# Kernel optimization log

Measured on AMD Instinct MI355X. Metric: run time of the kernel, lower is better.

Reference implementation:

```python
import jax
jax.config.update("jax_enable_x64", True)  # Sinkhorn runs in f64, matching torch's d.double()
import jax.numpy as jnp
import numpy as np

N, D, K = 32768, 128, 1024
TAU = 0.2
SK_EPS = 0.005
SK_ITERS = 3


def setup_inputs() -> dict:
    key = jax.random.key(0)
    k1, k2 = jax.random.split(key)
    x = jax.random.normal(k1, (N, D), dtype=jnp.float32)
    codebook = jax.random.normal(k2, (K, D), dtype=jnp.float32) * 0.02  # embedding.weight
    return {"x": x, "codebook": codebook}


def _l2norm(v):
    # F.normalize with eps=1e-12
    n = jnp.linalg.norm(v, axis=-1, keepdims=True)
    return v / jnp.maximum(n, 1e-12)


def _center_distance(d):
    d = jnp.where(jnp.isnan(d), jnp.zeros_like(d), d)
    mx, mn = d.max(), d.min()
    middle = (mx + mn) / 2
    amplitude = jnp.maximum(mx - middle + 1e-5, 1e-5)
    return (d - middle) / amplitude


def _sinkhorn(d, epsilon, iters):
    # d: [N, K] in f64; Q: [K, N]
    Q = jnp.exp(-d / epsilon).T
    Kc, B = Q.shape
    Q = Q / jnp.maximum(Q.sum(), 1e-5)

    def body(Q, _):
        Q = Q / Q.sum(axis=1, keepdims=True) / Kc
        Q = Q / Q.sum(axis=0, keepdims=True) / B
        return Q, None

    Q, _ = jax.lax.scan(body, Q, None, length=iters)
    return (Q * B).T  # [N, K]


def reference(x, codebook):
    latent = x.reshape(-1, codebook.shape[-1])  # [N, D]
    cos_sim = _l2norm(latent) @ _l2norm(codebook).T  # [N, K]
    d = (1.0 - cos_sim) / TAU

    # training path with sk_epsilon > 0: center + Sinkhorn (no_grad in torch)
    dc = _center_distance(jax.lax.stop_gradient(d))
    Q = _sinkhorn(dc.astype(jnp.float64), SK_EPS, SK_ITERS)
    indices = jnp.argmax(Q, axis=-1)  # [N]

    x_q = codebook[indices].reshape(x.shape)

    # cross-entropy(cos_sim / tau, indices.detach())
    logits = cos_sim / TAU
    logp = jax.nn.log_softmax(logits, axis=-1)
    loss = -jnp.mean(jnp.take_along_axis(logp, indices[:, None], axis=-1))

    # straight-through estimator
    x_q = x + jax.lax.stop_gradient(x_q - x)
    return x_q, loss, indices
```

## Files before the change

kernel.cpp:

```cpp
#include <hip/hip_runtime.h>
#include <cstddef>

#define NPTS 32768
#define DDIM 128
#define KCB  1024

typedef __attribute__((ext_vector_type(8))) short short8;
typedef __attribute__((ext_vector_type(4))) float f32x4;


__device__ __forceinline__ float hw_exp2(float x) {
#if __has_builtin(__builtin_amdgcn_exp2f)
  return __builtin_amdgcn_exp2f(x);
#else
  return exp2f(x);
#endif
}

__device__ __forceinline__ void atomic_add_f64(double* p, double v) {
  __hip_atomic_fetch_add(p, v, __ATOMIC_RELAXED, __HIP_MEMORY_SCOPE_AGENT);
}

__device__ __forceinline__ unsigned short bf16_rne(float v) {
  unsigned u = __float_as_uint(v);
  unsigned r = u + 0x7FFFu + ((u >> 16) & 1u);
  return (unsigned short)(r >> 16);
}
__device__ __forceinline__ float bf16_tof(unsigned short h) {
  return __uint_as_float((unsigned)h << 16);
}

__device__ __forceinline__ float div_mark(float x, float c, float rc) {
  float q0 = x * rc;
  float r  = fmaf(-c, q0, x);
  return fmaf(r, rc, q0);
}

__device__ __forceinline__ double sweep_E(float cv, float middle, float amp, float rc_amp) {
  float d  = div_mark(1.0f - cv, 0.2f, 1.0f / 0.2f);
  float dc = div_mark(d - middle, amp, rc_amp);
  double xl2 = (double)dc * (-288.53900817779268);
  double kd  = rint(xl2);
  float  fr  = (float)(xl2 - kd);
  float  m   = hw_exp2(fr);
  long long bits = ((long long)(1023 + (int)kd)) << 52;
  return (double)m * __longlong_as_double(bits);
}

__device__ __forceinline__ double score_exponent(float cv, float middle, float amplitude) {
  float d  = (1.0f - cv) / 0.2f;
  float dc = (d - middle) / amplitude;
  return (double)dc * (-(1.0 / 0.005));
}

__device__ __forceinline__ unsigned enc_f32(float f) {
  unsigned u = __float_as_uint(f);
  return (u & 0x80000000u) ? ~u : (u | 0x80000000u);
}
__device__ __forceinline__ float dec_f32(unsigned e) {
  unsigned u = (e & 0x80000000u) ? (e & 0x7FFFFFFFu) : ~e;
  return __uint_as_float(u);
}

__device__ __forceinline__ void calc_scal(const unsigned* maxenc, const unsigned* minenc,
                                          float& middle, float& amplitude, float& rc_amp) {
  float cosmax = dec_f32(*maxenc);
  float cosmin = dec_f32(*minenc);
  float mx_d = (1.0f - cosmin) / 0.2f;
  float mn_d = (1.0f - cosmax) / 0.2f;
  middle = (mx_d + mn_d) / 2.0f;
  amplitude = fmaxf(mx_d - middle + 1e-5f, 1e-5f);
  rc_amp = 1.0f / amplitude;
}

#if __has_builtin(__builtin_amdgcn_global_load_lds)
#define HAVE_ASYNC_LDS 1
typedef __attribute__((address_space(3))) unsigned int lds_u32_t;
typedef const __attribute__((address_space(1))) unsigned int glb_u32_t;
__device__ __forceinline__ void async_ld16(const void* g, void* l) {
  __builtin_amdgcn_global_load_lds((glb_u32_t*)g, (lds_u32_t*)l, 16, 0, 0);
}
#else
#define HAVE_ASYNC_LDS 0
#endif

#define WAITVM8() asm volatile("s_waitcnt vmcnt(8)" ::: "memory")
#define WAITVM4() asm volatile("s_waitcnt vmcnt(4)" ::: "memory")
#define WAITVM0() asm volatile("s_waitcnt vmcnt(0)" ::: "memory")
#define CFENCE()  asm volatile("" ::: "memory")
#define SBAR()    do { CFENCE(); __builtin_amdgcn_s_barrier(); CFENCE(); } while (0)


__global__ __launch_bounds__(1024) void vq_init_kernel(double* __restrict__ u123,
                                                       double* __restrict__ loss_part,
                                                       unsigned* __restrict__ maxenc,
                                                       unsigned* __restrict__ minenc) {
  int t = threadIdx.x;
  for (int i = t; i < 3 * KCB; i += 1024) u123[i] = 0.0;
  loss_part[t] = 0.0;
  if (t == 0) {
    *maxenc = 0u;
    *minenc = 0xFFFFFFFFu;
  }
}

__global__ __launch_bounds__(128) void vq_normalize_rows(const float* __restrict__ in,
                                                         float* __restrict__ out) {
  int row = blockIdx.x;
  int t = threadIdx.x;
  float v = in[(size_t)row * DDIM + t];
  float s = v * v;
#pragma unroll
  for (int off = 32; off; off >>= 1) s += __shfl_down(s, off, 64);
  __shared__ float red[2];
  if ((t & 63) == 0) red[t >> 6] = s;
  __syncthreads();
  float norm = sqrtf(red[0] + red[1]);
  out[(size_t)row * DDIM + t] = v / fmaxf(norm, 1e-12f);
}

__global__ __launch_bounds__(128) void vq_normalize_split(const float* __restrict__ in,
                                                          unsigned short* __restrict__ oh,
                                                          unsigned short* __restrict__ ol) {
  int row = blockIdx.x;
  int t = threadIdx.x;
  float v = in[(size_t)row * DDIM + t];
  float s = v * v;
#pragma unroll
  for (int off = 32; off; off >>= 1) s += __shfl_down(s, off, 64);
  __shared__ float red[2];
  if ((t & 63) == 0) red[t >> 6] = s;
  __syncthreads();
  float norm = sqrtf(red[0] + red[1]);
  float xnv = v / fmaxf(norm, 1e-12f);
  unsigned short h = bf16_rne(xnv);
  float fh = bf16_tof(h);
  unsigned short l = bf16_rne(xnv - fh);
  size_t idx = (size_t)row * DDIM + t;
  oh[idx] = h;
  ol[idx] = l;
}


__global__ __launch_bounds__(512, 2) void vq_gemm_mfma(const unsigned short* __restrict__ Ah,
                                                       const unsigned short* __restrict__ Al,
                                                       const unsigned short* __restrict__ Bh,
                                                       const unsigned short* __restrict__ Bl,
                                                       float* __restrict__ Cm,
                                                       unsigned* __restrict__ maxenc,
                                                       unsigned* __restrict__ minenc) {
  __shared__ unsigned short Ab[4][8192];
  __shared__ unsigned short Bb[4][8192];
  __shared__ float redmx[8], redmn[8];
  int tid = threadIdx.x;
  int lane = tid & 63, wv = tid >> 6;
  int wm = wv >> 2, wn = wv & 3;
  int n0 = blockIdx.x * 256;
  int c0 = blockIdx.y * 256;
  int fr = lane & 15;
  int swz8 = (((lane >> 4) ^ ((lane >> 1) & 3))) * 8;
  int arow = (wm * 128 + fr) * 32 + swz8;
  int brow = (wn * 64 + fr) * 32 + swz8;
  int srcj8 = (((tid & 3) ^ ((tid >> 3) & 3))) * 8;
  int r0 = tid >> 2;
  f32x4 acc[8][4] = {};

  auto stageA = [&](int t) {
    const unsigned short* p = ((t & 3) < 2) ? Ah : Al;
    const unsigned short* g = p + (size_t)(n0 + r0) * DDIM + (t >> 2) * 32 + srcj8;
    unsigned short* lb = &Ab[t & 3][wv * 512];
#if HAVE_ASYNC_LDS
    async_ld16(g, lb);
    async_ld16(g + (size_t)128 * DDIM, lb + 4096);
#else
    *(short8*)(&Ab[t & 3][tid * 8])        = *(const short8*)g;
    *(short8*)(&Ab[t & 3][4096 + tid * 8]) = *(const short8*)(g + (size_t)128 * DDIM);
#endif
  };
  auto stageB = [&](int t) {
    const unsigned short* p = (t & 1) ? Bl : Bh;
    const unsigned short* g = p + (size_t)(c0 + r0) * DDIM + (t >> 2) * 32 + srcj8;
    unsigned short* lb = &Bb[t & 3][wv * 512];
#if HAVE_ASYNC_LDS
    async_ld16(g, lb);
    async_ld16(g + (size_t)128 * DDIM, lb + 4096);
#else
    *(short8*)(&Bb[t & 3][tid * 8])        = *(const short8*)g;
    *(short8*)(&Bb[t & 3][4096 + tid * 8]) = *(const short8*)(g + (size_t)128 * DDIM);
#endif
  };

  stageA(0); stageB(0);
  stageA(1); stageB(1);
  stageA(2); stageB(2);
  WAITVM8();
  SBAR();

  short8 af[4], bf[4];
#pragma unroll
  for (int t = 0; t < 16; ++t) {
    const unsigned short* ab = &Ab[t & 3][0];
    const unsigned short* bb = &Bb[t & 3][0];
#pragma unroll
    for (int ct = 0; ct < 4; ++ct) bf[ct] = *(const short8*)(bb + brow + ct * 512);
#pragma unroll
    for (int rt = 0; rt < 4; ++rt) af[rt] = *(const short8*)(ab + arow + rt * 512);
    if (t <= 12) stageA(t + 3);
    SBAR();
    __builtin_amdgcn_s_setprio(1);
#pragma unroll
    for (int rt = 0; rt < 4; ++rt)
#pragma unroll
      for (int ct = 0; ct < 4; ++ct)
        acc[rt][ct] = __builtin_amdgcn_mfma_f32_16x16x32_bf16(af[rt], bf[ct], acc[rt][ct], 0, 0, 0);
    __builtin_amdgcn_s_setprio(0);
    SBAR();
#pragma unroll
    for (int rt = 0; rt < 4; ++rt) af[rt] = *(const short8*)(ab + arow + (rt + 4) * 512);
    if (t <= 12) stageB(t + 3);
    SBAR();
    __builtin_amdgcn_s_setprio(1);
#pragma unroll
    for (int rt = 0; rt < 4; ++rt)
#pragma unroll
      for (int ct = 0; ct < 4; ++ct)
        acc[rt + 4][ct] = __builtin_amdgcn_mfma_f32_16x16x32_bf16(af[rt], bf[ct], acc[rt + 4][ct], 0, 0, 0);
    __builtin_amdgcn_s_setprio(0);
    if (t <= 12) WAITVM8();
    else if (t == 13) WAITVM4();
    else if (t == 14) WAITVM0();
    SBAR();
  }

  float mx = -3.402823466e38f, mn = 3.402823466e38f;
  int orow = (lane >> 4) * 4, ocol = lane & 15;
  int rn0 = n0 + wm * 128, rc0 = c0 + wn * 64;
#pragma unroll
  for (int rt = 0; rt < 8; ++rt) {
#pragma unroll
    for (int ct = 0; ct < 4; ++ct) {
#pragma unroll
      for (int r = 0; r < 4; ++r) {
        float v = acc[rt][ct][r];
        mx = fmaxf(mx, v);
        mn = fminf(mn, v);
        Cm[(size_t)(rn0 + rt * 16 + orow + r) * KCB + (rc0 + ct * 16 + ocol)] = v;
      }
    }
  }
#pragma unroll
  for (int off = 32; off; off >>= 1) {
    mx = fmaxf(mx, __shfl_down(mx, off, 64));
    mn = fminf(mn, __shfl_down(mn, off, 64));
  }
  if (lane == 0) { redmx[wv] = mx; redmn[wv] = mn; }
  __syncthreads();
  if (tid == 0) {
#pragma unroll
    for (int w = 1; w < 8; ++w) {
      mx = fmaxf(mx, redmx[w]);
      mn = fminf(mn, redmn[w]);
    }
    mx = fmaxf(mx, redmx[0]);
    mn = fminf(mn, redmn[0]);
    atomicMax(maxenc, enc_f32(mx));
    atomicMin(minenc, enc_f32(mn));
  }
}

#define SROWS 32
#define SRPW  8

__global__ __launch_bounds__(256) void vq_sweep(const float* __restrict__ Cm,
                                                const unsigned* __restrict__ maxenc,
                                                const unsigned* __restrict__ minenc,
                                                const double* __restrict__ Rvec,
                                                const double* __restrict__ alpha_p,
                                                double* __restrict__ u_out) {
  int t = threadIdx.x;
  int lane = t & 63, wv = t >> 6;
  int n0 = blockIdx.x * SROWS + wv * SRPW;
  float middle, amp, rc;
  calc_scal(maxenc, minenc, middle, amp, rc);
  bool hasR = (Rvec != nullptr);
  double Rreg[16];
  double ainv = 0.0;
  if (hasR) {
#pragma unroll
    for (int c = 0; c < 4; ++c)
#pragma unroll
      for (int e = 0; e < 4; ++e) Rreg[c * 4 + e] = Rvec[c * 256 + lane * 4 + e];
    ainv = alpha_p[0] * 32768.0;
  }
  double up[16] = {};
  float4 cva[4], cvb[4];
  {
    const float4* row0 = (const float4*)(Cm + (size_t)n0 * KCB);
#pragma unroll
    for (int c = 0; c < 4; ++c) cva[c] = row0[c * 64 + lane];
  }
#pragma unroll 1
  for (int r = 0; r < SRPW; ++r) {
    int rn = (r < SRPW - 1) ? r + 1 : r;
    const float4* rown = (const float4*)(Cm + (size_t)(n0 + rn) * KCB);
#pragma unroll
    for (int c = 0; c < 4; ++c) cvb[c] = rown[c * 64 + lane];
    double e[16];
#pragma unroll
    for (int c = 0; c < 4; ++c) {
      e[c * 4 + 0] = sweep_E(cva[c].x, middle, amp, rc);
      e[c * 4 + 1] = sweep_E(cva[c].y, middle, amp, rc);
      e[c * 4 + 2] = sweep_E(cva[c].z, middle, amp, rc);
      e[c * 4 + 3] = sweep_E(cva[c].w, middle, amp, rc);
    }
    if (hasR) {
      double s = 0.0;
#pragma unroll
      for (int i = 0; i < 16; ++i) s += e[i] * Rreg[i];
#pragma unroll
      for (int off = 1; off < 64; off <<= 1) s += __shfl_xor(s, off, 64);
      double C = 1.0 / (ainv * s);
#pragma unroll
      for (int i = 0; i < 16; ++i) up[i] += e[i] * C;
    } else {
#pragma unroll
      for (int i = 0; i < 16; ++i) up[i] += e[i];
    }
#pragma unroll
    for (int c = 0; c < 4; ++c) cva[c] = cvb[c];
  }
  __shared__ double su[4][KCB];
#pragma unroll
  for (int c = 0; c < 4; ++c)
#pragma unroll
    for (int e = 0; e < 4; ++e) su[wv][c * 256 + lane * 4 + e] = up[c * 4 + e];
  __syncthreads();
#pragma unroll
  for (int j = 0; j < 4; ++j) {
    int k = (t + ((blockIdx.x + j) & 3) * 256) & (KCB - 1);
    double v = su[0][k] + su[1][k] + su[2][k] + su[3][k];
    atomic_add_f64(&u_out[k], v);
  }
}

__global__ __launch_bounds__(1024) void vq_finalize_u(const double* __restrict__ u,
                                                      double* __restrict__ alpha_p,
                                                      double* __restrict__ R,
                                                      double* __restrict__ lnR,
                                                      int mode) {
  int k = threadIdx.x;
  double uk = u[k];
  __shared__ double red[16];
  __shared__ double s_alpha;
  if (mode == 0) {
    double s = uk;
#pragma unroll
    for (int off = 32; off; off >>= 1) s += __shfl_down(s, off, 64);
    if ((k & 63) == 0) red[k >> 6] = s;
    __syncthreads();
    if (k == 0) {
      double s0 = 0.0;
      for (int w = 0; w < 16; ++w) s0 += red[w];
      double a = 1.0 / fmax(s0, 1e-5);
      s_alpha = a;
      alpha_p[0] = a;
    }
    __syncthreads();
  }
  double alpha = (mode == 0) ? s_alpha : alpha_p[0];
  double r = 1.0 / (alpha * 1024.0 * uk);
  R[k] = r;
  if (mode == 2) lnR[k] = log(r);
}

#define FRPW 4
#define MARGIN 0.08f
#define LOG2E 1.44269504088896340736f

__global__ __launch_bounds__(256) void vq_final_pass(const float* __restrict__ Cm,
                                                     const float* __restrict__ x,
                                                     const float* __restrict__ cb,
                                                     const float* __restrict__ xn,
                                                     const float* __restrict__ cn,
                                                     const double* __restrict__ lnR,
                                                     const unsigned* __restrict__ maxenc,
                                                     const unsigned* __restrict__ minenc,
                                                     double* __restrict__ loss_part,
                                                     float* __restrict__ out_xq,
                                                     float* __restrict__ out_idx) {
  int t = threadIdx.x;
  int lane = t & 63, wv = t >> 6;
  int n0 = blockIdx.x * (4 * FRPW) + wv * FRPW;
  float middle, amplitude, rc_amp;
  calc_scal(maxenc, minenc, middle, amplitude, rc_amp);
  float lnRf[16];
#pragma unroll
  for (int c = 0; c < 4; ++c)
#pragma unroll
    for (int e = 0; e < 4; ++e)
      lnRf[c * 4 + e] = (float)lnR[c * 256 + lane * 4 + e];

  double loss_loc = 0.0;
  float4 cva[4], cvb[4];
  {
    const float4* row0 = (const float4*)(Cm + (size_t)n0 * KCB);
#pragma unroll
    for (int c = 0; c < 4; ++c) cva[c] = row0[c * 64 + lane];
  }
#pragma unroll 1
  for (int r = 0; r < FRPW; ++r) {
    int n = n0 + r;
    int rn = (r < FRPW - 1) ? r + 1 : r;
    const float4* rown = (const float4*)(Cm + (size_t)(n0 + rn) * KCB);
#pragma unroll
    for (int c = 0; c < 4; ++c) cvb[c] = rown[c * 64 + lane];

    float lv[16];
    float sv[16];
    float b1 = -3.402823466e38f, b2 = -3.402823466e38f;
    int k1 = 0;
    float lmax = -3.402823466e38f;
#pragma unroll
    for (int c = 0; c < 4; ++c) {
#pragma unroll
      for (int e = 0; e < 4; ++e) {
        float cvv = (e == 0) ? cva[c].x : (e == 1) ? cva[c].y : (e == 2) ? cva[c].z : cva[c].w;
        int k = c * 256 + lane * 4 + e;
        float d  = div_mark(1.0f - cvv, 0.2f, 5.0f);
        float dc = div_mark(d - middle, amplitude, rc_amp);
        float s  = fmaf(dc, -200.0f, lnRf[c * 4 + e]);
        sv[c * 4 + e] = s;
        if (s > b1) { b2 = b1; b1 = s; k1 = k; }
        else if (s > b2) b2 = s;
        float l = div_mark(cvv, 0.2f, 5.0f);
        lv[c * 4 + e] = l;
        lmax = fmaxf(lmax, l);
      }
    }
#pragma unroll
    for (int off = 1; off < 64; off <<= 1) {
      float o1 = __shfl_xor(b1, off, 64);
      int ok = __shfl_xor(k1, off, 64);
      float o2 = __shfl_xor(b2, off, 64);
      float om = __shfl_xor(lmax, off, 64);
      float cand2;
      if (o1 > b1 || (o1 == b1 && ok < k1)) { cand2 = fmaxf(b1, o2); b1 = o1; k1 = ok; }
      else cand2 = fmaxf(o1, o2);
      b2 = fmaxf(b2, cand2);
      lmax = fmaxf(lmax, om);
    }
    int bestk = k1;
    if (b1 - b2 < MARGIN) {
      double pbest = -1.0e308;
      int pk = KCB;
      const float4* xr4 = (const float4*)(xn + (size_t)n * DDIM);
      float thr = b1 - MARGIN;
#pragma unroll
      for (int i = 0; i < 16; ++i) {
        if (sv[i] >= thr) {
          int k = (i >> 2) * 256 + lane * 4 + (i & 3);
          const float4* cr4 = (const float4*)(cn + (size_t)k * DDIM);
          float dot = 0.0f;
#pragma unroll 4
          for (int d = 0; d < DDIM / 4; ++d) {
            float4 xv4 = xr4[d];
            float4 cv4 = cr4[d];
            dot = fmaf(xv4.x, cv4.x, dot);
            dot = fmaf(xv4.y, cv4.y, dot);
            dot = fmaf(xv4.z, cv4.z, dot);
            dot = fmaf(xv4.w, cv4.w, dot);
          }
          double ps = score_exponent(dot, middle, amplitude) + lnR[k];
          if (ps > pbest || (ps == pbest && k < pk)) { pbest = ps; pk = k; }
        }
      }
#pragma unroll
      for (int off = 1; off < 64; off <<= 1) {
        double ob = __shfl_xor(pbest, off, 64);
        int ok = __shfl_xor(pk, off, 64);
        if (ob > pbest || (ob == pbest && ok < pk)) { pbest = ob; pk = ok; }
      }
      bestk = pk;
    }
    float se = 0.0f;
    float lb = 0.0f;
#pragma unroll
    for (int c = 0; c < 4; ++c) {
#pragma unroll
      for (int e = 0; e < 4; ++e) {
        int k = c * 256 + lane * 4 + e;
        se += hw_exp2((lv[c * 4 + e] - lmax) * LOG2E);
        if (k == bestk) lb = lv[c * 4 + e];
      }
    }
#pragma unroll
    for (int off = 1; off < 64; off <<= 1) {
      se += __shfl_xor(se, off, 64);
      lb += __shfl_xor(lb, off, 64);
    }
    loss_loc += (double)(-(lb - lmax - logf(se)));
    if (lane == 0) out_idx[n] = (float)bestk;
    float2 xv = *(const float2*)&x[(size_t)n * DDIM + lane * 2];
    float2 cbv = *(const float2*)&cb[(size_t)bestk * DDIM + lane * 2];
    float2 o;
    o.x = xv.x + (cbv.x - xv.x);
    o.y = xv.y + (cbv.y - xv.y);
    *(float2*)&out_xq[(size_t)n * DDIM + lane * 2] = o;
#pragma unroll
    for (int c = 0; c < 4; ++c) cva[c] = cvb[c];
  }
  if (lane == 0) atomic_add_f64(&loss_part[(blockIdx.x * 4 + wv) & (KCB - 1)], loss_loc);
}

__global__ __launch_bounds__(1024) void vq_loss_div(const double* __restrict__ lp,
                                                    float* __restrict__ out_loss) {
  int t = threadIdx.x;
  double s = lp[t];
#pragma unroll
  for (int off = 32; off; off >>= 1) s += __shfl_down(s, off, 64);
  __shared__ double red[16];
  if ((t & 63) == 0) red[t >> 6] = s;
  __syncthreads();
  if (t == 0) {
    double tot = 0.0;
    for (int w = 0; w < 16; ++w) tot += red[w];
    out_loss[0] = (float)(tot / 32768.0);
  }
}


extern "C" void kernel_launch(void* const* d_in, const int* in_sizes, int n_in,
                              void* d_out, int out_size, void* d_ws, size_t ws_size,
                              hipStream_t stream) {
  const float* x  = (const float*)d_in[0];
  const float* cb = (const float*)d_in[1];
  float* out = (float*)d_out;
  float* out_xq   = out;
  float* out_loss = out + (size_t)NPTS * DDIM;
  float* out_idx  = out + (size_t)NPTS * DDIM + 1;

  char* w = (char*)d_ws;
  unsigned short* xh = (unsigned short*)w;
  unsigned short* xl = xh + (size_t)NPTS * DDIM;
  unsigned short* ch = xl + (size_t)NPTS * DDIM;
  unsigned short* cl = ch + (size_t)KCB * DDIM;
  float* xn = (float*)w;
  float* cn = xn + (size_t)NPTS * DDIM;
  float* cosm = (float*)(w + (size_t)16896 * 1024);
  double* u1  = (double*)(cosm + (size_t)NPTS * KCB);
  double* u2  = u1 + KCB;
  double* u3  = u2 + KCB;
  double* R   = u3 + KCB;
  double* lnR = R + KCB;
  double* loss_part = lnR + KCB;
  double* alpha_p   = loss_part + KCB;
  unsigned* maxenc = (unsigned*)(alpha_p + 1);
  unsigned* minenc = maxenc + 1;

  vq_init_kernel<<<1, 1024, 0, stream>>>(u1, loss_part, maxenc, minenc);

  vq_normalize_split<<<NPTS, 128, 0, stream>>>(x, xh, xl);
  vq_normalize_split<<<KCB, 128, 0, stream>>>(cb, ch, cl);
  vq_gemm_mfma<<<dim3(NPTS / 256, KCB / 256), 512, 0, stream>>>(xh, xl, ch, cl, cosm,
                                                                maxenc, minenc);

  vq_normalize_rows<<<NPTS, 128, 0, stream>>>(x, xn);
  vq_normalize_rows<<<KCB, 128, 0, stream>>>(cb, cn);

  vq_sweep<<<NPTS / SROWS, 256, 0, stream>>>(cosm, maxenc, minenc, nullptr, alpha_p, u1);
  vq_finalize_u<<<1, 1024, 0, stream>>>(u1, alpha_p, R, lnR, 0);
  vq_sweep<<<NPTS / SROWS, 256, 0, stream>>>(cosm, maxenc, minenc, R, alpha_p, u2);
  vq_finalize_u<<<1, 1024, 0, stream>>>(u2, alpha_p, R, lnR, 1);
  vq_sweep<<<NPTS / SROWS, 256, 0, stream>>>(cosm, maxenc, minenc, R, alpha_p, u3);
  vq_finalize_u<<<1, 1024, 0, stream>>>(u3, alpha_p, R, lnR, 2);

  vq_final_pass<<<NPTS / (4 * FRPW), 256, 0, stream>>>(cosm, x, cb, xn, cn, lnR,
                                                       maxenc, minenc,
                                                       loss_part, out_xq, out_idx);
  vq_loss_div<<<1, 1024, 0, stream>>>(loss_part, out_loss);
}
```

Baseline: 304.6 us.

## Shrink GEMM tile to 128x128 with 256 threads and triple-buffered LDS

The split-bf16 cosine GEMM now uses 128x128 output tiles with 4 waves instead of 256x256 with 8 waves. The LDS ring drops from 4 stages to 3 and loads two stages ahead. Each iteration stages A and B together and runs a single MFMA block, which removes two of the three barriers per k-step. The aim is to fit more blocks per CU and cut sync overhead, at the cost of less operand reuse per block and more global/L2 traffic for the inputs.

```diff
diff --git a/kernel.cpp b/kernel.cpp
--- a/kernel.cpp
+++ b/kernel.cpp
@@ -84,7 +84,6 @@
 #define HAVE_ASYNC_LDS 0
 #endif
 
-#define WAITVM8() asm volatile("s_waitcnt vmcnt(8)" ::: "memory")
 #define WAITVM4() asm volatile("s_waitcnt vmcnt(4)" ::: "memory")
 #define WAITVM0() asm volatile("s_waitcnt vmcnt(0)" ::: "memory")
 #define CFENCE()  asm volatile("" ::: "memory")
@@ -142,71 +141,69 @@
 }
 
 
-__global__ __launch_bounds__(512, 2) void vq_gemm_mfma(const unsigned short* __restrict__ Ah,
+__global__ __launch_bounds__(256, 3) void vq_gemm_mfma(const unsigned short* __restrict__ Ah,
                                                        const unsigned short* __restrict__ Al,
                                                        const unsigned short* __restrict__ Bh,
                                                        const unsigned short* __restrict__ Bl,
                                                        float* __restrict__ Cm,
                                                        unsigned* __restrict__ maxenc,
                                                        unsigned* __restrict__ minenc) {
-  __shared__ unsigned short Ab[4][8192];
-  __shared__ unsigned short Bb[4][8192];
-  __shared__ float redmx[8], redmn[8];
+  __shared__ unsigned short Ab[3][4096];
+  __shared__ unsigned short Bb[3][4096];
+  __shared__ float redmx[4], redmn[4];
   int tid = threadIdx.x;
   int lane = tid & 63, wv = tid >> 6;
-  int wm = wv >> 2, wn = wv & 3;
-  int n0 = blockIdx.x * 256;
-  int c0 = blockIdx.y * 256;
+  int wm = wv >> 1, wn = wv & 1;
+  int n0 = blockIdx.x * 128;
+  int c0 = blockIdx.y * 128;
   int fr = lane & 15;
   int swz8 = (((lane >> 4) ^ ((lane >> 1) & 3))) * 8;
-  int arow = (wm * 128 + fr) * 32 + swz8;
+  int arow = (wm * 64 + fr) * 32 + swz8;
   int brow = (wn * 64 + fr) * 32 + swz8;
   int srcj8 = (((tid & 3) ^ ((tid >> 3) & 3))) * 8;
   int r0 = tid >> 2;
-  f32x4 acc[8][4] = {};
+  f32x4 acc[4][4] = {};
 
   auto stageA = [&](int t) {
     const unsigned short* p = ((t & 3) < 2) ? Ah : Al;
     const unsigned short* g = p + (size_t)(n0 + r0) * DDIM + (t >> 2) * 32 + srcj8;
-    unsigned short* lb = &Ab[t & 3][wv * 512];
 #if HAVE_ASYNC_LDS
+    unsigned short* lb = &Ab[t % 3][wv * 512];
     async_ld16(g, lb);
-    async_ld16(g + (size_t)128 * DDIM, lb + 4096);
+    async_ld16(g + (size_t)64 * DDIM, lb + 2048);
 #else
-    *(short8*)(&Ab[t & 3][tid * 8])        = *(const short8*)g;
-    *(short8*)(&Ab[t & 3][4096 + tid * 8]) = *(const short8*)(g + (size_t)128 * DDIM);
+    *(short8*)(&Ab[t % 3][tid * 8])        = *(const short8*)g;
+    *(short8*)(&Ab[t % 3][2048 + tid * 8]) = *(const short8*)(g + (size_t)64 * DDIM);
 #endif
   };
   auto stageB = [&](int t) {
     const unsigned short* p = (t & 1) ? Bl : Bh;
     const unsigned short* g = p + (size_t)(c0 + r0) * DDIM + (t >> 2) * 32 + srcj8;
-    unsigned short* lb = &Bb[t & 3][wv * 512];
 #if HAVE_ASYNC_LDS
+    unsigned short* lb = &Bb[t % 3][wv * 512];
     async_ld16(g, lb);
-    async_ld16(g + (size_t)128 * DDIM, lb + 4096);
+    async_ld16(g + (size_t)64 * DDIM, lb + 2048);
 #else
-    *(short8*)(&Bb[t & 3][tid * 8])        = *(const short8*)g;
-    *(short8*)(&Bb[t & 3][4096 + tid * 8]) = *(const short8*)(g + (size_t)128 * DDIM);
+    *(short8*)(&Bb[t % 3][tid * 8])        = *(const short8*)g;
+    *(short8*)(&Bb[t % 3][2048 + tid * 8]) = *(const short8*)(g + (size_t)64 * DDIM);
 #endif
   };
 
   stageA(0); stageB(0);
   stageA(1); stageB(1);
-  stageA(2); stageB(2);
-  WAITVM8();
+  WAITVM4();
   SBAR();
 
   short8 af[4], bf[4];
 #pragma unroll
   for (int t = 0; t < 16; ++t) {
-    const unsigned short* ab = &Ab[t & 3][0];
-    const unsigned short* bb = &Bb[t & 3][0];
+    const unsigned short* ab = &Ab[t % 3][0];
+    const unsigned short* bb = &Bb[t % 3][0];
 #pragma unroll
     for (int ct = 0; ct < 4; ++ct) bf[ct] = *(const short8*)(bb + brow + ct * 512);
 #pragma unroll
     for (int rt = 0; rt < 4; ++rt) af[rt] = *(const short8*)(ab + arow + rt * 512);
-    if (t <= 12) stageA(t + 3);
-    SBAR();
+    if (t <= 13) { stageA(t + 2); stageB(t + 2); }
     __builtin_amdgcn_s_setprio(1);
 #pragma unroll
     for (int rt = 0; rt < 4; ++rt)
@@ -214,29 +211,16 @@
       for (int ct = 0; ct < 4; ++ct)
         acc[rt][ct] = __builtin_amdgcn_mfma_f32_16x16x32_bf16(af[rt], bf[ct], acc[rt][ct], 0, 0, 0);
     __builtin_amdgcn_s_setprio(0);
-    SBAR();
-#pragma unroll
-    for (int rt = 0; rt < 4; ++rt) af[rt] = *(const short8*)(ab + arow + (rt + 4) * 512);
-    if (t <= 12) stageB(t + 3);
-    SBAR();
-    __builtin_amdgcn_s_setprio(1);
-#pragma unroll
-    for (int rt = 0; rt < 4; ++rt)
-#pragma unroll
-      for (int ct = 0; ct < 4; ++ct)
-        acc[rt + 4][ct] = __builtin_amdgcn_mfma_f32_16x16x32_bf16(af[rt], bf[ct], acc[rt + 4][ct], 0, 0, 0);
-    __builtin_amdgcn_s_setprio(0);
-    if (t <= 12) WAITVM8();
-    else if (t == 13) WAITVM4();
+    if (t <= 13) WAITVM4();
     else if (t == 14) WAITVM0();
-    SBAR();
+    if (t < 15) SBAR();
   }
 
   float mx = -3.402823466e38f, mn = 3.402823466e38f;
   int orow = (lane >> 4) * 4, ocol = lane & 15;
-  int rn0 = n0 + wm * 128, rc0 = c0 + wn * 64;
-#pragma unroll
-  for (int rt = 0; rt < 8; ++rt) {
+  int rn0 = n0 + wm * 64, rc0 = c0 + wn * 64;
+#pragma unroll
+  for (int rt = 0; rt < 4; ++rt) {
 #pragma unroll
     for (int ct = 0; ct < 4; ++ct) {
 #pragma unroll
@@ -256,13 +240,8 @@
   if (lane == 0) { redmx[wv] = mx; redmn[wv] = mn; }
   __syncthreads();
   if (tid == 0) {
-#pragma unroll
-    for (int w = 1; w < 8; ++w) {
-      mx = fmaxf(mx, redmx[w]);
-      mn = fminf(mn, redmn[w]);
-    }
-    mx = fmaxf(mx, redmx[0]);
-    mn = fminf(mn, redmn[0]);
+    mx = fmaxf(fmaxf(redmx[0], redmx[1]), fmaxf(redmx[2], redmx[3]));
+    mn = fminf(fminf(redmn[0], redmn[1]), fminf(redmn[2], redmn[3]));
     atomicMax(maxenc, enc_f32(mx));
     atomicMin(minenc, enc_f32(mn));
   }
@@ -561,7 +540,7 @@
 
   vq_normalize_split<<<NPTS, 128, 0, stream>>>(x, xh, xl);
   vq_normalize_split<<<KCB, 128, 0, stream>>>(cb, ch, cl);
-  vq_gemm_mfma<<<dim3(NPTS / 256, KCB / 256), 512, 0, stream>>>(xh, xl, ch, cl, cosm,
+  vq_gemm_mfma<<<dim3(NPTS / 128, KCB / 128), 256, 0, stream>>>(xh, xl, ch, cl, cosm,
                                                                 maxenc, minenc);
 
   vq_normalize_rows<<<NPTS, 128, 0, stream>>>(x, xn);
```

New measurement: 320.7 us. 5.3% more time.
